# Kernel optimization log

Hardware: AMD Instinct MI355X
Metric: run time of the kernel (lower is better)

Reference implementation:

```python
import jax, jax.numpy as jnp
import numpy as np

N_EVENTS = 16384   # original pixel events
D = 128            # input_size
H = 128            # hidden_size
K = 9              # kernel 3x3 -> patch coords
S = 2048           # number of patch sequences
LMAX = 108         # max sequence length
T = 147456         # total patch events = sum(lengths) = 9 * N_EVENTS


def setup_inputs() -> dict:
    key = jax.random.key(0)
    ks = jax.random.split(key, 8)
    events = jax.random.normal(ks[0], (N_EVENTS, D), jnp.float32)
    pos_id = jax.random.randint(ks[1], (T,), 0, K, dtype=jnp.int32)
    orig_event_idx = jax.random.randint(ks[2], (T,), 0, N_EVENTS, dtype=jnp.int32)
    # alternating 36/108 lengths: 1024*36 + 1024*108 = 147456 = T
    lengths = jnp.where(jnp.arange(S) % 2 == 0, 36, 108).astype(jnp.int32)
    std = float(np.sqrt(2.0 / (D + H)))
    scatter_w = jax.random.normal(ks[3], (K, H, D), jnp.float32) * std
    gather_w = jax.random.normal(ks[4], (K, H, H), jnp.float32) * std
    lstm_std = float(1.0 / np.sqrt(H))
    w_ih = jax.random.uniform(ks[5], (4 * H, H), jnp.float32, -lstm_std, lstm_std)
    w_hh = jax.random.uniform(ks[6], (4 * H, H), jnp.float32, -lstm_std, lstm_std)
    ln_g = jnp.ones((H,), jnp.float32)
    ln_b = jnp.zeros((H,), jnp.float32)
    return dict(events=events, scatter_w=scatter_w, gather_w=gather_w,
                w_ih=w_ih, w_hh=w_hh, ln_g=ln_g, ln_b=ln_b,
                pos_id=pos_id, orig_event_idx=orig_event_idx, lengths=lengths)


def _pos_proj(x, W, pos_id):
    # position-indexed projection: out[t] = W[pos_id[t]] @ x[t]
    # loop over small fixed K=9 with masked accumulate (matches the torch loop)
    out = jnp.zeros((x.shape[0], W.shape[1]), x.dtype)
    for k in range(W.shape[0]):
        out = out + jnp.where((pos_id == k)[:, None], x @ W[k].T, 0.0)
    return out


def reference(events, scatter_w, gather_w, w_ih, w_hh, ln_g, ln_b,
              pos_id, orig_event_idx, lengths):
    # scatter events to patch replicas
    x = events[orig_event_idx]                           # [T, D]
    x = _pos_proj(x, scatter_w, pos_id)                  # [T, H]

    # flat (sequence-major) -> padded [S, LMAX, H]
    seq_offsets = jnp.cumsum(lengths) - lengths          # [S]
    seq_ids = jnp.repeat(jnp.arange(S), lengths, total_repeat_length=T)
    pos_in_seq = jnp.arange(T) - seq_offsets[seq_ids]
    padded = jnp.zeros((S, LMAX, H), x.dtype).at[seq_ids, pos_in_seq].set(x)

    # single-layer bias-free LSTM (pytorch gate order i, f, g, o), zero init.
    # zero-padding after each sequence's valid region leaves valid outputs
    # identical to a PackedSequence LSTM.
    def step(carry, xt):                                 # xt: [S, H]
        h, c = carry
        gates = xt @ w_ih.T + h @ w_hh.T                 # [S, 4H]
        i, f, g, o = jnp.split(gates, 4, axis=-1)
        c = jax.nn.sigmoid(f) * c + jax.nn.sigmoid(i) * jnp.tanh(g)
        h = jax.nn.sigmoid(o) * jnp.tanh(c)
        return (h, c), h

    init = (jnp.zeros((S, H), x.dtype), jnp.zeros((S, H), x.dtype))
    _, hs = jax.lax.scan(step, init, jnp.swapaxes(padded, 0, 1))  # [LMAX, S, H]
    o_flat = jnp.swapaxes(hs, 0, 1)[seq_ids, pos_in_seq]          # [T, H]

    o_flat = _pos_proj(o_flat, gather_w, pos_id)                  # [T, H]

    # gather patch events back to pixel events (scatter-add) + residual + LN
    out = jnp.zeros((N_EVENTS, H), x.dtype).at[orig_event_idx].add(o_flat)
    out = out + events                                   # input_proj is None (D == H)
    mu = jnp.mean(out, axis=-1, keepdims=True)
    var = jnp.var(out, axis=-1, keepdims=True)
    out = (out - mu) * jax.lax.rsqrt(var + 1e-5) * ln_g + ln_b
    return out
```

## Files before the change

kernel.cpp:

```cpp
#include <hip/hip_runtime.h>

#define N_EVENTS 16384
#define DIM 128
#define NK 9
#define NSEQ 2048
#define TT 147456
#define CHUNK 64
#define NCHUNK_MAX (TT/CHUNK + NK)
#define NHBLK 576

typedef __attribute__((ext_vector_type(8))) short bf16x8;
typedef __attribute__((ext_vector_type(4))) float f32x4;
typedef __attribute__((ext_vector_type(4))) int i32x4;
typedef __attribute__((ext_vector_type(2))) int i32x2;

#define OFF_EV     0UL
#define OFF_WC     (OFF_EV   + (size_t)N_EVENTS*DIM*2)
#define OFF_SCAT   (OFF_WC   + (size_t)512*256*2)
#define OFF_GATH   (OFF_SCAT + (size_t)NK*DIM*DIM*2)
#define OFF_XS     (OFF_GATH + (size_t)NK*DIM*DIM*2)
#define OFF_HS     (OFF_XS   + (size_t)TT*DIM*2)
#define OFF_KLIST  (OFF_HS   + (size_t)TT*DIM*2)
#define OFF_ECNT   (OFF_KLIST+ (size_t)TT*4)
#define OFF_EOFF   (OFF_ECNT + 16384UL*4)
#define OFF_ECNT2  (OFF_EOFF + 16392UL*4)
#define OFF_ELIST  (OFF_ECNT2+ 16384UL*4)
#define OFF_SEQOFF (OFF_ELIST+ (size_t)TT*4)
#define OFF_GROUP  (OFF_SEQOFF + (size_t)NSEQ*4)
#define OFF_MISC   (OFF_GROUP  + (size_t)NSEQ*4)
#define OFF_BH     (OFF_MISC   + 256UL)

__device__ __forceinline__ short f2b(float f) {
    union { float f; unsigned u; } v; v.f = f;
    unsigned r = (v.u + 0x7FFFu + ((v.u >> 16) & 1u)) >> 16;
    return (short)r;
}
__device__ __forceinline__ float asf(unsigned u) {
    union { unsigned u; float f; } v; v.u = u; return v.f;
}
__device__ __forceinline__ float fsig(float x) {
    return __builtin_amdgcn_rcpf(1.f + __expf(-x));
}
__device__ __forceinline__ float ftanh(float x) {
    return 1.f - 2.f * __builtin_amdgcn_rcpf(__expf(2.f * x) + 1.f);
}

__device__ __forceinline__ float plo(float a, float b) {
    i32x2 r = __builtin_amdgcn_permlane32_swap(__float_as_int(a), __float_as_int(b),
                                               false, false);
    return __int_as_float(r[0]);
}

__device__ __forceinline__ void wg_bar_nodrain() {
    __builtin_amdgcn_sched_barrier(0);
    asm volatile("s_waitcnt lgkmcnt(0)");
    __builtin_amdgcn_s_barrier();
    __builtin_amdgcn_sched_barrier(0);
}

__global__ void convert_kernel(const float* __restrict__ ev, const float* __restrict__ wih,
                               const float* __restrict__ whh, const float* __restrict__ sw,
                               const float* __restrict__ gw,
                               short* __restrict__ evb, short* __restrict__ wcb,
                               short* __restrict__ swb, short* __restrict__ gwb,
                               int* __restrict__ ecnt, int* __restrict__ ecnt2) {
    int idx = blockIdx.x * blockDim.x + threadIdx.x;
    if (idx < N_EVENTS * DIM) evb[idx] = f2b(ev[idx]);
    if (idx < 512 * DIM) {
        int j = idx >> 7, d = idx & 127;
        wcb[j * 256 + d]       = f2b(wih[idx]);
        wcb[j * 256 + 128 + d] = f2b(whh[idx]);
    }
    if (idx < NK * DIM * DIM) { swb[idx] = f2b(sw[idx]); gwb[idx] = f2b(gw[idx]); }
    if (idx < N_EVENTS) { ecnt[idx] = 0; ecnt2[idx] = 0; }
}

__global__ void hist_kernel(const int* __restrict__ pos, const int* __restrict__ orig,
                            int* __restrict__ blockhist, int* __restrict__ ecnt) {
    __shared__ int h[NK];
    int tid = threadIdx.x;
    if (tid < NK) h[tid] = 0;
    __syncthreads();
    int t = blockIdx.x * 256 + tid;
    atomicAdd(&h[pos[t]], 1);
    atomicAdd(&ecnt[orig[t]], 1);
    __syncthreads();
    if (tid < NK) blockhist[blockIdx.x * NK + tid] = h[tid];
}

__global__ void plan_kernel(int* __restrict__ blockhist, int* __restrict__ misc,
                            const int* __restrict__ lengths, int* __restrict__ seq_off,
                            int* __restrict__ grouped,
                            const int* __restrict__ ecnt, int* __restrict__ eoff) {
    int tid = threadIdx.x;
    if (blockIdx.x == 0) {
        __shared__ int h[NHBLK * NK];
        for (int i = tid; i < NHBLK * NK; i += 256) h[i] = blockhist[i];
        __syncthreads();
        if (tid < NK) {
            int run = 0;
            for (int b = 0; b < NHBLK; b++) {
                int v = h[b * NK + tid];
                h[b * NK + tid] = run;
                run += v;
            }
            misc[tid] = run;
        }
        __syncthreads();
        if (tid == 0) {
            int ko = 0, co = 0;
            for (int k = 0; k < NK; k++) {
                int c = misc[k];
                misc[32 + k] = ko;
                misc[48 + k] = co;
                ko += c;
                co += (c + CHUNK - 1) / CHUNK;
            }
            misc[48 + NK] = co;
        }
        __syncthreads();
        for (int i = tid; i < NHBLK * NK; i += 256) blockhist[i] = h[i];
    } else if (blockIdx.x == 1) {
        __shared__ int lens[NSEQ];
        __shared__ int tsum[256], tlong[256];
        for (int i = tid; i < NSEQ; i += 256) lens[i] = lengths[i];
        __syncthreads();
        int base = tid * 8;
        int ls[8]; int s = 0, lc = 0;
        #pragma unroll
        for (int i = 0; i < 8; i++) { ls[i] = lens[base + i]; s += ls[i]; lc += (ls[i] > 64) ? 1 : 0; }
        tsum[tid] = s; tlong[tid] = lc;
        __syncthreads();
        for (int d = 1; d < 256; d <<= 1) {
            int a = (tid >= d) ? tsum[tid - d] : 0;
            int b = (tid >= d) ? tlong[tid - d] : 0;
            __syncthreads();
            tsum[tid] += a; tlong[tid] += b;
            __syncthreads();
        }
        int nlong_total = tlong[255];
        int excl = tsum[tid] - s;
        int excl_long = tlong[tid] - lc;
        int run = 0, runl = 0;
        #pragma unroll
        for (int i = 0; i < 8; i++) {
            int sid = base + i;
            seq_off[sid] = excl + run;
            int lb = excl_long + runl;
            if (ls[i] > 64) { grouped[lb] = sid; runl++; }
            else            { grouped[nlong_total + (sid - lb)] = sid; }
            run += ls[i];
        }
    } else {
        __shared__ int part[256];
        int base = tid * 64;
        int s = 0;
        for (int j = 0; j < 64; j++) s += ecnt[base + j];
        part[tid] = s;
        __syncthreads();
        for (int d = 1; d < 256; d <<= 1) {
            int a = (tid >= d) ? part[tid - d] : 0;
            __syncthreads();
            part[tid] += a;
            __syncthreads();
        }
        int run = part[tid] - s;
        for (int j = 0; j < 64; j++) {
            eoff[base + j] = run;
            run += ecnt[base + j];
        }
        if (tid == 255) eoff[N_EVENTS] = run;
    }
}

__global__ void fill_kernel(const int* __restrict__ pos, const int* __restrict__ orig,
                            const int* __restrict__ blockhist, const int* __restrict__ misc,
                            int* __restrict__ klist,
                            const int* __restrict__ eoff, int* __restrict__ ecnt2,
                            int* __restrict__ elist) {
    __shared__ int off[NK];
    int tid = threadIdx.x;
    if (tid < NK) off[tid] = misc[32 + tid] + blockhist[blockIdx.x * NK + tid];
    __syncthreads();
    int t = blockIdx.x * 256 + tid;
    int p = atomicAdd(&off[pos[t]], 1);
    klist[p] = t;
    int o = orig[t];
    int p2 = atomicAdd(&ecnt2[o], 1);
    elist[eoff[o] + p2] = t;
}

__global__ void bucket_gemm(const short* __restrict__ src, const short* __restrict__ wall,
                            const int* __restrict__ klist, const int* __restrict__ misc,
                            const int* __restrict__ orig, short* __restrict__ rows_out,
                            int mode) {
    const int* chunkoff = misc + 48;
    int b = blockIdx.x;
    if (b >= chunkoff[NK]) return;
    int k = 0;
    while (k < NK - 1 && chunkoff[k + 1] <= b) k++;
    int lc = b - chunkoff[k];
    int cnt = misc[k];
    int base = misc[32 + k] + lc * CHUNK;
    int nv = min(CHUNK, cnt - lc * CHUNK);

    __shared__ int tok[CHUNK], ridx[CHUNK];
    __shared__ short A[CHUNK * 136];
    int tid = threadIdx.x;
    if (tid < CHUNK) {
        int tv = klist[base + ((tid < nv) ? tid : 0)];
        tok[tid] = tv;
        ridx[tid] = (mode == 0) ? orig[tv] : tv;
    }
    __syncthreads();
    {
        int row = tid >> 2, part = tid & 3;
        const i32x4* s4 = (const i32x4*)(src + (size_t)ridx[row] * DIM + part * 32);
        i32x4* d4 = (i32x4*)(A + row * 136 + part * 32);
        d4[0] = s4[0]; d4[1] = s4[1]; d4[2] = s4[2]; d4[3] = s4[3];
    }
    __syncthreads();
    int wave = tid >> 6, lane = tid & 63, l15 = lane & 15, q = lane >> 4;
    const short* wk = wall + (size_t)k * DIM * DIM;
    bf16x8 Bf[2][4];
    #pragma unroll
    for (int nt = 0; nt < 2; nt++) {
        int h = wave * 32 + nt * 16 + l15;
        #pragma unroll
        for (int kt = 0; kt < 4; kt++)
            Bf[nt][kt] = *(const bf16x8*)(wk + h * DIM + kt * 32 + q * 8);
    }
    f32x4 C[4][2];
    #pragma unroll
    for (int mt = 0; mt < 4; mt++)
        #pragma unroll
        for (int nt = 0; nt < 2; nt++) C[mt][nt] = (f32x4){0.f, 0.f, 0.f, 0.f};
    #pragma unroll
    for (int mt = 0; mt < 4; mt++) {
        bf16x8 Afr[4];
        const short* ar = A + (mt * 16 + l15) * 136 + q * 8;
        Afr[0] = *(const bf16x8*)(ar);
        Afr[1] = *(const bf16x8*)(ar + 32);
        Afr[2] = *(const bf16x8*)(ar + 64);
        Afr[3] = *(const bf16x8*)(ar + 96);
        #pragma unroll
        for (int nt = 0; nt < 2; nt++)
            #pragma unroll
            for (int kt = 0; kt < 4; kt++)
                C[mt][nt] = __builtin_amdgcn_mfma_f32_16x16x32_bf16(Afr[kt], Bf[nt][kt], C[mt][nt], 0, 0, 0);
    }
    __syncthreads();
    #pragma unroll
    for (int mt = 0; mt < 4; mt++)
        #pragma unroll
        for (int nt = 0; nt < 2; nt++)
            #pragma unroll
            for (int r = 0; r < 4; r++) {
                int row = mt * 16 + q * 4 + r;
                int col = wave * 32 + nt * 16 + l15;
                A[row * 136 + col] = f2b(C[mt][nt][r]);
            }
    __syncthreads();
    {
        int row = tid >> 2, part = tid & 3;
        if (row < nv) {
            const i32x4* s4 = (const i32x4*)(A + row * 136 + part * 32);
            i32x4* d4 = (i32x4*)(rows_out + (size_t)tok[row] * DIM + part * 32);
            d4[0] = s4[0]; d4[1] = s4[1]; d4[2] = s4[2]; d4[3] = s4[3];
        }
    }
}

#define MF(a, b, c) __builtin_amdgcn_mfma_f32_16x16x32_bf16(a, b, c, 0, 0, 0)

#define LSTM_STEP(J, PF) { \
    const int i_ = ib8 + (J); \
    f32x4 Ci = {0.f,0.f,0.f,0.f}, Cf = {0.f,0.f,0.f,0.f}; \
    f32x4 Cg = {0.f,0.f,0.f,0.f}, Co = {0.f,0.f,0.f,0.f}; \
    Ci = MF(PF[0], Bf[0][0], Ci); Cf = MF(PF[0], Bf[1][0], Cf); \
    Cg = MF(PF[0], Bf[2][0], Cg); Co = MF(PF[0], Bf[3][0], Co); \
    Ci = MF(PF[1], Bf[0][1], Ci); Cf = MF(PF[1], Bf[1][1], Cf); \
    Cg = MF(PF[1], Bf[2][1], Cg); Co = MF(PF[1], Bf[3][1], Co); \
    Ci = MF(PF[2], Bf[0][2], Ci); Cf = MF(PF[2], Bf[1][2], Cf); \
    Cg = MF(PF[2], Bf[2][2], Cg); Co = MF(PF[2], Bf[3][2], Co); \
    Ci = MF(PF[3], Bf[0][3], Ci); Cf = MF(PF[3], Bf[1][3], Cf); \
    Cg = MF(PF[3], Bf[2][3], Cg); Co = MF(PF[3], Bf[3][3], Co); \
    bf16x8 Hf0, Hf1, Hf2, Hf3; \
    { const short* hp_ = hb + (((J) + 7) & 7) * 1088 + l15 * 136 + ql * 8; \
      Hf0 = *(const bf16x8*)(hp_);      Hf1 = *(const bf16x8*)(hp_ + 32); \
      Hf2 = *(const bf16x8*)(hp_ + 64); Hf3 = *(const bf16x8*)(hp_ + 96); } \
    Ci = MF(Hf0, Bf[0][4], Ci); Cf = MF(Hf0, Bf[1][4], Cf); \
    Cg = MF(Hf0, Bf[2][4], Cg); Co = MF(Hf0, Bf[3][4], Co); \
    Ci = MF(Hf1, Bf[0][5], Ci); Cf = MF(Hf1, Bf[1][5], Cf); \
    Cg = MF(Hf1, Bf[2][5], Cg); Co = MF(Hf1, Bf[3][5], Co); \
    Ci = MF(Hf2, Bf[0][6], Ci); Cf = MF(Hf2, Bf[1][6], Cf); \
    Cg = MF(Hf2, Bf[2][6], Cg); Co = MF(Hf2, Bf[3][6], Co); \
    Ci = MF(Hf3, Bf[0][7], Ci); Cf = MF(Hf3, Bf[1][7], Cf); \
    Cg = MF(Hf3, Bf[2][7], Cg); Co = MF(Hf3, Bf[3][7], Co); \
    if (l15 < 8) { \
        const short* xp_ = xs + xoff; \
        PF[0] = *(const bf16x8*)(xp_);      PF[1] = *(const bf16x8*)(xp_ + 32); \
        PF[2] = *(const bf16x8*)(xp_ + 64); PF[3] = *(const bf16x8*)(xp_ + 96); \
    } \
    xoff += ((i_ + 4) <= my_len) ? DIM : 0; \
    { \
        float iA = plo(Ci[0], Ci[2]), iB = plo(Ci[1], Ci[3]); \
        float fA = plo(Cf[0], Cf[2]), fB = plo(Cf[1], Cf[3]); \
        float gA = plo(Cg[0], Cg[2]), gB = plo(Cg[1], Cg[3]); \
        float oA = plo(Co[0], Co[2]), oB = plo(Co[1], Co[3]); \
        if (i_ < lenA) { \
            float si = fsig(iA), sf = fsig(fA), so = fsig(oA); \
            float tg = ftanh(gA); \
            float cn = sf * cA + si * tg; \
            float th = ftanh(cn); \
            cA = cn; \
            hb[(J) * 1088 + rowA * 136 + u] = f2b(so * th); \
        } \
        if (i_ < lenB) { \
            float si = fsig(iB), sf = fsig(fB), so = fsig(oB); \
            float tg = ftanh(gB); \
            float cn = sf * cB + si * tg; \
            float th = ftanh(cn); \
            cB = cn; \
            hb[(J) * 1088 + rowB * 136 + u] = f2b(so * th); \
        } \
    } \
    wg_bar_nodrain(); \
}

__global__ __launch_bounds__(512, 2) void lstm_kernel(
        const short* __restrict__ xs, const short* __restrict__ wc,
        short* __restrict__ hstore, const int* __restrict__ seq_off,
        const int* __restrict__ grouped, const int* __restrict__ lengths) {
    __shared__ int s_off[8], s_len[8];
    __shared__ short hchunk[11][8][136];
    int tid = threadIdx.x;
    if (tid < 8) {
        int s = grouped[blockIdx.x * 8 + tid];
        s_off[tid] = seq_off[s];
        s_len[tid] = lengths[s];
    }
    for (int j = tid; j < 11 * 8 * 136; j += 512) ((short*)hchunk)[j] = 0;
    __syncthreads();
    int lane = tid & 63, l15 = lane & 15, ql = lane >> 4;
    int wave = tid >> 6;
    int u = wave * 16 + l15;
    short* hb = (short*)hchunk;
    bf16x8 Bf[4][8];
    #pragma unroll
    for (int g = 0; g < 4; g++) {
        int j = g * 128 + u;
        #pragma unroll
        for (int kt = 0; kt < 8; kt++)
            Bf[g][kt] = *(const bf16x8*)(wc + j * 256 + kt * 32 + ql * 8);
    }
    int maxlen = 0;
    #pragma unroll
    for (int i = 0; i < 8; i++) maxlen = max(maxlen, s_len[i]);
    int my_off = (l15 < 8) ? s_off[l15] : 0;
    int my_len = (l15 < 8) ? s_len[l15] : 1;
    int rowA = (ql < 2) ? (ql * 4 + 0) : ((ql - 2) * 4 + 2);
    int rowB = (ql < 2) ? (ql * 4 + 1) : ((ql - 2) * 4 + 3);
    int lenA = s_len[rowA], lenB = s_len[rowB];
    float cA = 0.f, cB = 0.f;
    bf16x8 Pf0[4], Pf1[4];
    #pragma unroll
    for (int k = 0; k < 4; k++) { Pf0[k] = (bf16x8){0,0,0,0,0,0,0,0}; Pf1[k] = Pf0[k]; }
    int xoff = my_off * DIM + ql * 8;
    if (l15 < 8) {
        const short* xp = xs + xoff;
        Pf0[0] = *(const bf16x8*)(xp);      Pf0[1] = *(const bf16x8*)(xp + 32);
        Pf0[2] = *(const bf16x8*)(xp + 64); Pf0[3] = *(const bf16x8*)(xp + 96);
    }
    int xoff1 = xoff + ((my_len > 1) ? DIM : 0);
    if (l15 < 8) {
        const short* xp = xs + xoff1;
        Pf1[0] = *(const bf16x8*)(xp);      Pf1[1] = *(const bf16x8*)(xp + 32);
        Pf1[2] = *(const bf16x8*)(xp + 64); Pf1[3] = *(const bf16x8*)(xp + 96);
    }
    xoff = xoff1 + ((my_len > 2) ? DIM : 0);

    int nb8 = (maxlen + 7) >> 3;
    for (int ob = 0; ob < nb8; ob++) {
        int ib8 = ob * 8;
        LSTM_STEP(0, Pf0)
        LSTM_STEP(1, Pf1)
        LSTM_STEP(2, Pf0)
        LSTM_STEP(3, Pf1)
        LSTM_STEP(4, Pf0)
        LSTM_STEP(5, Pf1)
        LSTM_STEP(6, Pf0)
        LSTM_STEP(7, Pf1)
        #pragma unroll
        for (int it = 0; it < 2; it++) {
            int idx = tid + it * 512;
            int st = idx >> 7, s = (idx >> 4) & 7, part = idx & 15;
            int ig = ib8 + st;
            if (ig < s_len[s]) {
                i32x4 v = *(const i32x4*)&hchunk[st][s][part * 8];
                *(i32x4*)(hstore + (size_t)(s_off[s] + ig) * DIM + part * 8) = v;
            }
        }
        wg_bar_nodrain();
    }
}

__global__ void gather_ln(const short* __restrict__ of, const int* __restrict__ eoff,
                          const int* __restrict__ elist, const float* __restrict__ ev,
                          const float* __restrict__ g, const float* __restrict__ bta,
                          float* __restrict__ out) {
    int tid = threadIdx.x;
    int wave = tid >> 6, lane = tid & 63;
    int e = blockIdx.x * 4 + wave;
    int s0 = eoff[e], s1 = eoff[e + 1];
    float x0 = 0.f, x1 = 0.f;
    for (int j = s0; j < s1; j++) {
        int t = elist[j];
        unsigned v = *(const unsigned*)(of + (size_t)t * DIM + lane * 2);
        x0 += asf(v << 16);
        x1 += asf(v & 0xffff0000u);
    }
    const float2* e2 = (const float2*)(ev + (size_t)e * DIM);
    float2 evv = e2[lane];
    x0 += evv.x; x1 += evv.y;
    float sm = x0 + x1, sq = x0 * x0 + x1 * x1;
    #pragma unroll
    for (int m = 1; m < 64; m <<= 1) {
        sm += __shfl_xor(sm, m, 64);
        sq += __shfl_xor(sq, m, 64);
    }
    float mean = sm * (1.f / DIM);
    float var = sq * (1.f / DIM) - mean * mean;
    float rs = rsqrtf(var + 1e-5f);
    float2 gv = ((const float2*)g)[lane], bv = ((const float2*)bta)[lane];
    float2 ov;
    ov.x = (x0 - mean) * rs * gv.x + bv.x;
    ov.y = (x1 - mean) * rs * gv.y + bv.y;
    ((float2*)(out + (size_t)e * DIM))[lane] = ov;
}

extern "C" void kernel_launch(void* const* d_in, const int* in_sizes, int n_in,
                              void* d_out, int out_size, void* d_ws, size_t ws_size,
                              hipStream_t stream) {
    const float* events = (const float*)d_in[0];
    const float* scat   = (const float*)d_in[1];
    const float* gath   = (const float*)d_in[2];
    const float* wih    = (const float*)d_in[3];
    const float* whh    = (const float*)d_in[4];
    const float* lng    = (const float*)d_in[5];
    const float* lnb    = (const float*)d_in[6];
    const int* posid    = (const int*)d_in[7];
    const int* orig     = (const int*)d_in[8];
    const int* lens     = (const int*)d_in[9];
    char* ws = (char*)d_ws;
    short* evb   = (short*)(ws + OFF_EV);
    short* wcb   = (short*)(ws + OFF_WC);
    short* swb   = (short*)(ws + OFF_SCAT);
    short* gwb   = (short*)(ws + OFF_GATH);
    short* xs    = (short*)(ws + OFF_XS);
    short* hs    = (short*)(ws + OFF_HS);
    int*   klist = (int*)(ws + OFF_KLIST);
    int*   ecnt  = (int*)(ws + OFF_ECNT);
    int*   eoff  = (int*)(ws + OFF_EOFF);
    int*   ecnt2 = (int*)(ws + OFF_ECNT2);
    int*   elist = (int*)(ws + OFF_ELIST);
    int*   seqo  = (int*)(ws + OFF_SEQOFF);
    int*   grp   = (int*)(ws + OFF_GROUP);
    int*   misc  = (int*)(ws + OFF_MISC);
    int*   bh    = (int*)(ws + OFF_BH);
    float* out   = (float*)d_out;

    convert_kernel<<<8192, 256, 0, stream>>>(events, wih, whh, scat, gath,
                                             evb, wcb, swb, gwb, ecnt, ecnt2);
    hist_kernel<<<NHBLK, 256, 0, stream>>>(posid, orig, bh, ecnt);
    plan_kernel<<<3, 256, 0, stream>>>(bh, misc, lens, seqo, grp, ecnt, eoff);
    fill_kernel<<<NHBLK, 256, 0, stream>>>(posid, orig, bh, misc, klist, eoff, ecnt2, elist);
    bucket_gemm<<<NCHUNK_MAX, 256, 0, stream>>>(evb, swb, klist, misc, orig, xs, 0);
    lstm_kernel<<<256, 512, 0, stream>>>(xs, wcb, hs, seqo, grp, lens);
    bucket_gemm<<<NCHUNK_MAX, 256, 0, stream>>>(hs, gwb, klist, misc, orig, xs, 1);
    gather_ln<<<4096, 256, 0, stream>>>(xs, eoff, elist, events, lng, lnb, out);
}
```

Before: 289.0 us.

## Software-pipeline LSTM input projection one step ahead of recurrent matmul

Restructures the LSTM step so the input-side MFMAs (x_t @ W_ih) for the next timestep are issued before the recurrent h @ W_hh MFMAs of the current step, using double-buffered gate accumulators. This takes the input projection off the serial critical path between barriers, so only the recurrent half depends on the previous h. It costs 16 extra accumulator registers and reorders the prefetch buffers, which could lower occupancy or add spills.

```diff
diff --git a/kernel.cpp b/kernel.cpp
--- a/kernel.cpp
+++ b/kernel.cpp
@@ -273,41 +273,41 @@
 
 #define MF(a, b, c) __builtin_amdgcn_mfma_f32_16x16x32_bf16(a, b, c, 0, 0, 0)
 
-#define LSTM_STEP(J, PF) { \
+#define LSTM_STEP2(J, PC, PN, IC, FC, GC, OC, IN, FN, GN, ON) { \
     const int i_ = ib8 + (J); \
-    f32x4 Ci = {0.f,0.f,0.f,0.f}, Cf = {0.f,0.f,0.f,0.f}; \
-    f32x4 Cg = {0.f,0.f,0.f,0.f}, Co = {0.f,0.f,0.f,0.f}; \
-    Ci = MF(PF[0], Bf[0][0], Ci); Cf = MF(PF[0], Bf[1][0], Cf); \
-    Cg = MF(PF[0], Bf[2][0], Cg); Co = MF(PF[0], Bf[3][0], Co); \
-    Ci = MF(PF[1], Bf[0][1], Ci); Cf = MF(PF[1], Bf[1][1], Cf); \
-    Cg = MF(PF[1], Bf[2][1], Cg); Co = MF(PF[1], Bf[3][1], Co); \
-    Ci = MF(PF[2], Bf[0][2], Ci); Cf = MF(PF[2], Bf[1][2], Cf); \
-    Cg = MF(PF[2], Bf[2][2], Cg); Co = MF(PF[2], Bf[3][2], Co); \
-    Ci = MF(PF[3], Bf[0][3], Ci); Cf = MF(PF[3], Bf[1][3], Cf); \
-    Cg = MF(PF[3], Bf[2][3], Cg); Co = MF(PF[3], Bf[3][3], Co); \
     bf16x8 Hf0, Hf1, Hf2, Hf3; \
     { const short* hp_ = hb + (((J) + 7) & 7) * 1088 + l15 * 136 + ql * 8; \
       Hf0 = *(const bf16x8*)(hp_);      Hf1 = *(const bf16x8*)(hp_ + 32); \
       Hf2 = *(const bf16x8*)(hp_ + 64); Hf3 = *(const bf16x8*)(hp_ + 96); } \
-    Ci = MF(Hf0, Bf[0][4], Ci); Cf = MF(Hf0, Bf[1][4], Cf); \
-    Cg = MF(Hf0, Bf[2][4], Cg); Co = MF(Hf0, Bf[3][4], Co); \
-    Ci = MF(Hf1, Bf[0][5], Ci); Cf = MF(Hf1, Bf[1][5], Cf); \
-    Cg = MF(Hf1, Bf[2][5], Cg); Co = MF(Hf1, Bf[3][5], Co); \
-    Ci = MF(Hf2, Bf[0][6], Ci); Cf = MF(Hf2, Bf[1][6], Cf); \
-    Cg = MF(Hf2, Bf[2][6], Cg); Co = MF(Hf2, Bf[3][6], Co); \
-    Ci = MF(Hf3, Bf[0][7], Ci); Cf = MF(Hf3, Bf[1][7], Cf); \
-    Cg = MF(Hf3, Bf[2][7], Cg); Co = MF(Hf3, Bf[3][7], Co); \
     if (l15 < 8) { \
         const short* xp_ = xs + xoff; \
-        PF[0] = *(const bf16x8*)(xp_);      PF[1] = *(const bf16x8*)(xp_ + 32); \
-        PF[2] = *(const bf16x8*)(xp_ + 64); PF[3] = *(const bf16x8*)(xp_ + 96); \
+        PN[0] = *(const bf16x8*)(xp_);      PN[1] = *(const bf16x8*)(xp_ + 32); \
+        PN[2] = *(const bf16x8*)(xp_ + 64); PN[3] = *(const bf16x8*)(xp_ + 96); \
     } \
     xoff += ((i_ + 4) <= my_len) ? DIM : 0; \
+    IN = (f32x4){0.f,0.f,0.f,0.f}; FN = (f32x4){0.f,0.f,0.f,0.f}; \
+    GN = (f32x4){0.f,0.f,0.f,0.f}; ON = (f32x4){0.f,0.f,0.f,0.f}; \
+    IN = MF(PC[0], Bf[0][0], IN); FN = MF(PC[0], Bf[1][0], FN); \
+    GN = MF(PC[0], Bf[2][0], GN); ON = MF(PC[0], Bf[3][0], ON); \
+    IN = MF(PC[1], Bf[0][1], IN); FN = MF(PC[1], Bf[1][1], FN); \
+    GN = MF(PC[1], Bf[2][1], GN); ON = MF(PC[1], Bf[3][1], ON); \
+    IN = MF(PC[2], Bf[0][2], IN); FN = MF(PC[2], Bf[1][2], FN); \
+    GN = MF(PC[2], Bf[2][2], GN); ON = MF(PC[2], Bf[3][2], ON); \
+    IN = MF(PC[3], Bf[0][3], IN); FN = MF(PC[3], Bf[1][3], FN); \
+    GN = MF(PC[3], Bf[2][3], GN); ON = MF(PC[3], Bf[3][3], ON); \
+    IC = MF(Hf0, Bf[0][4], IC); FC = MF(Hf0, Bf[1][4], FC); \
+    GC = MF(Hf0, Bf[2][4], GC); OC = MF(Hf0, Bf[3][4], OC); \
+    IC = MF(Hf1, Bf[0][5], IC); FC = MF(Hf1, Bf[1][5], FC); \
+    GC = MF(Hf1, Bf[2][5], GC); OC = MF(Hf1, Bf[3][5], OC); \
+    IC = MF(Hf2, Bf[0][6], IC); FC = MF(Hf2, Bf[1][6], FC); \
+    GC = MF(Hf2, Bf[2][6], GC); OC = MF(Hf2, Bf[3][6], OC); \
+    IC = MF(Hf3, Bf[0][7], IC); FC = MF(Hf3, Bf[1][7], FC); \
+    GC = MF(Hf3, Bf[2][7], GC); OC = MF(Hf3, Bf[3][7], OC); \
     { \
-        float iA = plo(Ci[0], Ci[2]), iB = plo(Ci[1], Ci[3]); \
-        float fA = plo(Cf[0], Cf[2]), fB = plo(Cf[1], Cf[3]); \
-        float gA = plo(Cg[0], Cg[2]), gB = plo(Cg[1], Cg[3]); \
-        float oA = plo(Co[0], Co[2]), oB = plo(Co[1], Co[3]); \
+        float iA = plo(IC[0], IC[2]), iB = plo(IC[1], IC[3]); \
+        float fA = plo(FC[0], FC[2]), fB = plo(FC[1], FC[3]); \
+        float gA = plo(GC[0], GC[2]), gB = plo(GC[1], GC[3]); \
+        float oA = plo(OC[0], OC[2]), oB = plo(OC[1], OC[3]); \
         if (i_ < lenA) { \
             float si = fsig(iA), sf = fsig(fA), so = fsig(oA); \
             float tg = ftanh(gA); \
@@ -380,17 +380,29 @@
     }
     xoff = xoff1 + ((my_len > 2) ? DIM : 0);
 
+    f32x4 CiA = {0.f,0.f,0.f,0.f}, CfA = {0.f,0.f,0.f,0.f};
+    f32x4 CgA = {0.f,0.f,0.f,0.f}, CoA = {0.f,0.f,0.f,0.f};
+    f32x4 CiB, CfB, CgB, CoB;
+    CiA = MF(Pf0[0], Bf[0][0], CiA); CfA = MF(Pf0[0], Bf[1][0], CfA);
+    CgA = MF(Pf0[0], Bf[2][0], CgA); CoA = MF(Pf0[0], Bf[3][0], CoA);
+    CiA = MF(Pf0[1], Bf[0][1], CiA); CfA = MF(Pf0[1], Bf[1][1], CfA);
+    CgA = MF(Pf0[1], Bf[2][1], CgA); CoA = MF(Pf0[1], Bf[3][1], CoA);
+    CiA = MF(Pf0[2], Bf[0][2], CiA); CfA = MF(Pf0[2], Bf[1][2], CfA);
+    CgA = MF(Pf0[2], Bf[2][2], CgA); CoA = MF(Pf0[2], Bf[3][2], CoA);
+    CiA = MF(Pf0[3], Bf[0][3], CiA); CfA = MF(Pf0[3], Bf[1][3], CfA);
+    CgA = MF(Pf0[3], Bf[2][3], CgA); CoA = MF(Pf0[3], Bf[3][3], CoA);
+
     int nb8 = (maxlen + 7) >> 3;
     for (int ob = 0; ob < nb8; ob++) {
         int ib8 = ob * 8;
-        LSTM_STEP(0, Pf0)
-        LSTM_STEP(1, Pf1)
-        LSTM_STEP(2, Pf0)
-        LSTM_STEP(3, Pf1)
-        LSTM_STEP(4, Pf0)
-        LSTM_STEP(5, Pf1)
-        LSTM_STEP(6, Pf0)
-        LSTM_STEP(7, Pf1)
+        LSTM_STEP2(0, Pf1, Pf0, CiA,CfA,CgA,CoA, CiB,CfB,CgB,CoB)
+        LSTM_STEP2(1, Pf0, Pf1, CiB,CfB,CgB,CoB, CiA,CfA,CgA,CoA)
+        LSTM_STEP2(2, Pf1, Pf0, CiA,CfA,CgA,CoA, CiB,CfB,CgB,CoB)
+        LSTM_STEP2(3, Pf0, Pf1, CiB,CfB,CgB,CoB, CiA,CfA,CgA,CoA)
+        LSTM_STEP2(4, Pf1, Pf0, CiA,CfA,CgA,CoA, CiB,CfB,CgB,CoB)
+        LSTM_STEP2(5, Pf0, Pf1, CiB,CfB,CgB,CoB, CiA,CfA,CgA,CoA)
+        LSTM_STEP2(6, Pf1, Pf0, CiA,CfA,CgA,CoA, CiB,CfB,CgB,CoB)
+        LSTM_STEP2(7, Pf0, Pf1, CiB,CfB,CgB,CoB, CiA,CfA,CgA,CoA)
         #pragma unroll
         for (int it = 0; it < 2; it++) {
             int idx = tid + it * 512;
```

Measured after the change: 307.0 us. +6.2%, slower.
